# Performance work log

Measured on AMD Instinct MI355X. Metric: run time of the kernel, lower is better.

Reference implementation:

```python
import jax, jax.numpy as jnp
import numpy as np


def deform_conv2d(x, w, offset, mask, pad):
    """Modulated deformable conv (DCNv2), stride 1, dilation 1, groups 1.
    x: [B,C,H,W], w: [Co,C,kh,kw], offset: [B,2*K,H,W] (y,x per tap), mask: [B,K,H,W].
    Output spatial size equals input (pad = (k-1)//2).
    """
    B, C, H, W = x.shape
    Co, _, kh, kw = w.shape
    K = kh * kw
    off = offset.reshape(B, K, 2, H, W)
    dy, dx = off[:, :, 0], off[:, :, 1]               # [B,K,H,W]
    ky, kx = jnp.meshgrid(jnp.arange(kh), jnp.arange(kw), indexing='ij')
    ky = ky.reshape(K).astype(x.dtype)
    kx = kx.reshape(K).astype(x.dtype)
    hh = jnp.arange(H, dtype=x.dtype)
    ww = jnp.arange(W, dtype=x.dtype)
    # sampling coords: p0 + p_k + delta p_k
    py = hh[None, None, :, None] - pad + ky[None, :, None, None] + dy  # [B,K,H,W]
    px = ww[None, None, None, :] - pad + kx[None, :, None, None] + dx
    y0 = jnp.floor(py)
    x0 = jnp.floor(px)
    wy = py - y0
    wx = px - x0
    y0i = y0.astype(jnp.int32)
    x0i = x0.astype(jnp.int32)
    x_flat = x.reshape(B, C, H * W)

    def gather(yi, xi):
        valid = (yi >= 0) & (yi < H) & (xi >= 0) & (xi < W)  # zero padding outside
        idx = jnp.clip(yi, 0, H - 1) * W + jnp.clip(xi, 0, W - 1)
        g = jnp.take_along_axis(x_flat, idx.reshape(B, 1, K * H * W), axis=2)
        g = g.reshape(B, C, K, H, W)
        return g * valid[:, None].astype(x.dtype)

    v00 = gather(y0i, x0i)
    v01 = gather(y0i, x0i + 1)
    v10 = gather(y0i + 1, x0i)
    v11 = gather(y0i + 1, x0i + 1)
    wy_ = wy[:, None]  # [B,1,K,H,W]
    wx_ = wx[:, None]
    samp = (v00 * (1 - wy_) * (1 - wx_) + v01 * (1 - wy_) * wx_
            + v10 * wy_ * (1 - wx_) + v11 * wy_ * wx_)   # [B,C,K,H,W]
    # masked weighted accumulation == conv over sampled taps
    return jnp.einsum('bckhw,bkhw,ock->bohw', samp, mask, w.reshape(Co, C, K))


def setup_inputs() -> dict:
    key = jax.random.key(0)
    ks = jax.random.split(key, 10)
    B, C, H, W, Co = 4, 64, 64, 64, 64
    inp = {
        'x': jax.random.normal(ks[0], (B, C, H, W), dtype=jnp.float32),
        'filter1': jax.random.normal(ks[1], (Co, C, 3, 3), dtype=jnp.float32) * 0.05,
        'offset1': jax.random.normal(ks[2], (B, 2 * 9, H, W), dtype=jnp.float32),
        'mask1': jax.random.uniform(ks[3], (B, 9, H, W), dtype=jnp.float32),
        'filter2': jax.random.normal(ks[4], (Co, C, 5, 5), dtype=jnp.float32) * 0.03,
        'offset2': jax.random.normal(ks[5], (B, 2 * 25, H, W), dtype=jnp.float32),
        'mask2': jax.random.uniform(ks[6], (B, 25, H, W), dtype=jnp.float32),
        'filter3': jax.random.normal(ks[7], (Co, C, 7, 7), dtype=jnp.float32) * 0.02,
        'offset3': jax.random.normal(ks[8], (B, 2 * 49, H, W), dtype=jnp.float32),
        'mask3': jax.random.uniform(ks[9], (B, 49, H, W), dtype=jnp.float32),
    }
    return inp


def reference(x, filter1, offset1, mask1, filter2, offset2, mask2, filter3, offset3, mask3):
    part1 = deform_conv2d(x, filter1, offset1, mask1, pad=1)  # 3x3
    part2 = deform_conv2d(x, filter2, offset2, mask2, pad=2)  # 5x5
    part3 = deform_conv2d(x, filter3, offset3, mask3, pad=3)  # 7x7
    return jnp.concatenate((part1, part2, part3), axis=1)
```

## Files before the change

kernel.cpp:

```cpp
#include <hip/hip_runtime.h>
#include <hip/hip_bf16.h>


typedef __attribute__((ext_vector_type(8))) short bf16x8;
typedef __attribute__((ext_vector_type(8))) unsigned short u16x8;
typedef __attribute__((ext_vector_type(4))) float f32x4;
typedef __attribute__((ext_vector_type(2))) float f32x2;

#define WR 16
#define WC 30
#define WS 68
#define SLS 20

__device__ __forceinline__ unsigned short f2bf(float f) {
    __hip_bfloat16 h = __float2bfloat16(f);
    return *reinterpret_cast<unsigned short*>(&h);
}
__device__ __forceinline__ f32x2 unpk(unsigned u) {
    f32x2 r;
    r[0] = __uint_as_float(u << 16);
    r[1] = __uint_as_float(u & 0xffff0000u);
    return r;
}

__global__ __launch_bounds__(256) void k_prep(
    const float* __restrict__ x,
    const float* __restrict__ f1, const float* __restrict__ f2, const float* __restrict__ f3,
    unsigned short* __restrict__ xTb,
    unsigned short* __restrict__ wp1, unsigned short* __restrict__ wp2, unsigned short* __restrict__ wp3) {
    __shared__ float tile[64][65];
    int bid = blockIdx.x;
    int tid = threadIdx.x;
    if (bid < 256) {
        int b = bid >> 6, h = bid & 63;
        {
            int w = tid & 63, c4 = tid >> 6;
            const float* xp = x + (((b * 64) * 64 + h) * 64) + w;
            #pragma unroll
            for (int i = 0; i < 16; ++i) {
                int c = c4 * 16 + i;
                tile[c][w] = xp[c * 4096];
            }
        }
        __syncthreads();
        {
            int c = tid & 63, w4 = tid >> 6;
            unsigned short* op = xTb + (((b * 64 + h) * 64) * 64) + c;
            #pragma unroll
            for (int i = 0; i < 16; ++i) {
                int ww = w4 * 16 + i;
                op[ww * 64] = f2bf(tile[c][ww]);
            }
        }
    } else {
        int idx = (bid - 256) * 256 + tid;
        const float* f; unsigned short* wp; int K, rel;
        if (idx < 36864)       { f = f1; wp = wp1; K = 9;  rel = idx; }
        else if (idx < 139264) { f = f2; wp = wp2; K = 25; rel = idx - 36864; }
        else                   { f = f3; wp = wp3; K = 49; rel = idx - 139264; }
        int k    = rel >> 12;
        int r2   = rel & 4095;
        int ct   = r2 >> 10;
        int cg   = (r2 >> 9) & 1;
        int lane = (r2 >> 3) & 63;
        int j    = r2 & 7;
        int o = ct * 16 + (lane & 15);
        int c = cg * 32 + (lane >> 4) * 8 + j;
        wp[rel] = f2bf(f[(o * 64 + c) * K + k]);
    }
}

__global__ __launch_bounds__(512, 2) void k_dcn(
    const unsigned short* __restrict__ xTb,
    const float* __restrict__ off1, const float* __restrict__ msk1, const unsigned short* __restrict__ wp1,
    const float* __restrict__ off2, const float* __restrict__ msk2, const unsigned short* __restrict__ wp2,
    const float* __restrict__ off3, const float* __restrict__ msk3, const unsigned short* __restrict__ wp3,
    float* __restrict__ out) {

    __shared__ __align__(16) unsigned char smem[WR * WC * WS * 2];
    unsigned short* win = (unsigned short*)smem;
    float* slab = (float*)smem;

    int tile = blockIdx.x;
    int b  = tile >> 8;
    int h  = (tile >> 2) & 63;
    int w0 = (tile & 3) << 4;

    int tid  = threadIdx.x;
    int wv   = tid >> 6;
    int lane = tid & 63;
    int quad = lane >> 4;
    int l16  = lane & 15;
    int ylo  = h - 7, cxlo = w0 - 7;

    const unsigned short* xb = xTb + ((size_t)b << 18);

    int pw   = w0 + l16;
    int ch0  = quad << 3;
    int lofs = lane << 3;

    const float* offs; const float* msks; const unsigned short* wpF;
    int ks, ke, kw, pad;
    switch (wv) {
        case 0:  offs = off1; msks = msk1; wpF = wp1; kw = 3; pad = 1; ks = 0;  ke = 9;  break;
        case 1:  offs = off2; msks = msk2; wpF = wp2; kw = 5; pad = 2; ks = 0;  ke = 12; break;
        case 2:  offs = off2; msks = msk2; wpF = wp2; kw = 5; pad = 2; ks = 12; ke = 25; break;
        case 3:  offs = off3; msks = msk3; wpF = wp3; kw = 7; pad = 3; ks = 0;  ke = 10; break;
        case 4:  offs = off3; msks = msk3; wpF = wp3; kw = 7; pad = 3; ks = 10; ke = 20; break;
        case 5:  offs = off3; msks = msk3; wpF = wp3; kw = 7; pad = 3; ks = 20; ke = 30; break;
        case 6:  offs = off3; msks = msk3; wpF = wp3; kw = 7; pad = 3; ks = 30; ke = 40; break;
        default: offs = off3; msks = msk3; wpF = wp3; kw = 7; pad = 3; ks = 40; ke = 49; break;
    }
    int K2 = (kw == 3) ? 9 : (kw == 5) ? 25 : 49;
    const float* offp = offs + ((b * 2 * K2) * 4096) + (h << 6) + pw;
    const float* mskp = msks + ((b * K2) * 4096) + (h << 6) + pw;

    int kp1 = min(ks + 1, ke - 1), kp2 = min(ks + 2, ke - 1);
    float dyA = offp[ks * 8192], dxA = offp[ks * 8192 + 4096], mkA = mskp[ks * 4096];
    float dyB = offp[kp1 * 8192], dxB = offp[kp1 * 8192 + 4096], mkB = mskp[kp1 * 4096];
    float dyC = offp[kp2 * 8192], dxC = offp[kp2 * 8192 + 4096], mkC = mskp[kp2 * 4096];

    {
        int j = tid & 7;
        for (int p = tid >> 3; p < WR * WC; p += 64) {
            int r = p / WC, cc = p - r * WC;
            int y = min(max(ylo + r, 0), 63);
            int x = min(max(cxlo + cc, 0), 63);
            *(u16x8*)(win + p * WS + j * 8) =
                *(const u16x8*)(xb + (((y << 6) + x) << 6) + j * 8);
        }
    }
    __syncthreads();

    f32x4 acc[4];
    #pragma unroll
    for (int i = 0; i < 4; ++i) acc[i] = (f32x4){0.f, 0.f, 0.f, 0.f};

    int ky = ks / kw, kx = ks - ky * kw;

    for (int k = ks; k < ke; ++k) {
        const unsigned short* wpk = wpF + (k << 12) + lofs;
        bf16x8 b00 = *(const bf16x8*)(wpk);
        bf16x8 b01 = *(const bf16x8*)(wpk + 512);
        bf16x8 b10 = *(const bf16x8*)(wpk + 1024);
        bf16x8 b11 = *(const bf16x8*)(wpk + 1536);
        bf16x8 b20 = *(const bf16x8*)(wpk + 2048);
        bf16x8 b21 = *(const bf16x8*)(wpk + 2560);
        bf16x8 b30 = *(const bf16x8*)(wpk + 3072);
        bf16x8 b31 = *(const bf16x8*)(wpk + 3584);

        int kn = min(k + 3, ke - 1);
        float dyN = offp[kn * 8192];
        float dxN = offp[kn * 8192 + 4096];
        float mkN = mskp[kn * 4096];

        float py = (float)(h - pad + ky) + dyA;
        float px = (float)(pw - pad + kx) + dxA;
        float y0f = floorf(py), x0f = floorf(px);
        float wy = py - y0f, wx = px - x0f;
        int y0 = (int)y0f, x0 = (int)x0f;
        int y1 = y0 + 1, x1 = x0 + 1;
        float fy0 = ((unsigned)y0 < 64u) ? (1.f - wy) * mkA : 0.f;
        float fy1 = ((unsigned)y1 < 64u) ? wy * mkA         : 0.f;
        float gx0 = ((unsigned)x0 < 64u) ? (1.f - wx)       : 0.f;
        float gx1 = ((unsigned)x1 < 64u) ? wx               : 0.f;
        float w00 = fy0 * gx0, w01 = fy0 * gx1, w10 = fy1 * gx0, w11 = fy1 * gx1;

        int r0 = y0 - ylo, r1 = r0 + 1;
        int c0 = x0 - cxlo, c1 = c0 + 1;
        bool oow = ((w00 != 0.f) & (((unsigned)r0 >= WR) | ((unsigned)c0 >= WC)))
                 | ((w01 != 0.f) & (((unsigned)r0 >= WR) | ((unsigned)c1 >= WC)))
                 | ((w10 != 0.f) & (((unsigned)r1 >= WR) | ((unsigned)c0 >= WC)))
                 | ((w11 != 0.f) & (((unsigned)r1 >= WR) | ((unsigned)c1 >= WC)));
        int r0c = min(max(r0, 0), WR - 1), r1c = min(max(r1, 0), WR - 1);
        int c0c = min(max(c0, 0), WC - 1), c1c = min(max(c1, 0), WC - 1);
        int p00 = (r0c * WC + c0c) * WS;
        int p01 = (r0c * WC + c1c) * WS;
        int p10 = (r1c * WC + c0c) * WS;
        int p11 = (r1c * WC + c1c) * WS;

        union U { u16x8 v; unsigned u[4]; };
        U g00a, g01a, g10a, g11a, g00b, g01b, g10b, g11b;
        g00a.v = *(const u16x8*)(win + p00 + ch0);
        g01a.v = *(const u16x8*)(win + p01 + ch0);
        g10a.v = *(const u16x8*)(win + p10 + ch0);
        g11a.v = *(const u16x8*)(win + p11 + ch0);
        g00b.v = *(const u16x8*)(win + p00 + 32 + ch0);
        g01b.v = *(const u16x8*)(win + p01 + 32 + ch0);
        g10b.v = *(const u16x8*)(win + p10 + 32 + ch0);
        g11b.v = *(const u16x8*)(win + p11 + 32 + ch0);

        if (oow) {
            int y0g = min(max(y0, 0), 63), y1g = min(max(y1, 0), 63);
            int x0g = min(max(x0, 0), 63), x1g = min(max(x1, 0), 63);
            int o00 = ((y0g << 6) + x0g) << 6;
            int o01 = ((y0g << 6) + x1g) << 6;
            int o10 = ((y1g << 6) + x0g) << 6;
            int o11 = ((y1g << 6) + x1g) << 6;
            g00a.v = *(const u16x8*)(xb + o00 + ch0);
            g01a.v = *(const u16x8*)(xb + o01 + ch0);
            g10a.v = *(const u16x8*)(xb + o10 + ch0);
            g11a.v = *(const u16x8*)(xb + o11 + ch0);
            g00b.v = *(const u16x8*)(xb + o00 + 32 + ch0);
            g01b.v = *(const u16x8*)(xb + o01 + 32 + ch0);
            g10b.v = *(const u16x8*)(xb + o10 + 32 + ch0);
            g11b.v = *(const u16x8*)(xb + o11 + 32 + ch0);
        }

        f32x2 W00 = {w00, w00}, W01 = {w01, w01}, W10 = {w10, w10}, W11 = {w11, w11};
        union { bf16x8 v; unsigned short u[8]; } A0, A1;
        #pragma unroll
        for (int j2 = 0; j2 < 4; ++j2) {
            f32x2 s0 = W00 * unpk(g00a.u[j2]) + W01 * unpk(g01a.u[j2])
                     + W10 * unpk(g10a.u[j2]) + W11 * unpk(g11a.u[j2]);
            f32x2 s1 = W00 * unpk(g00b.u[j2]) + W01 * unpk(g01b.u[j2])
                     + W10 * unpk(g10b.u[j2]) + W11 * unpk(g11b.u[j2]);
            A0.u[2 * j2]     = f2bf(s0[0]);
            A0.u[2 * j2 + 1] = f2bf(s0[1]);
            A1.u[2 * j2]     = f2bf(s1[0]);
            A1.u[2 * j2 + 1] = f2bf(s1[1]);
        }

        acc[0] = __builtin_amdgcn_mfma_f32_16x16x32_bf16(A0.v, b00, acc[0], 0, 0, 0);
        acc[0] = __builtin_amdgcn_mfma_f32_16x16x32_bf16(A1.v, b01, acc[0], 0, 0, 0);
        acc[1] = __builtin_amdgcn_mfma_f32_16x16x32_bf16(A0.v, b10, acc[1], 0, 0, 0);
        acc[1] = __builtin_amdgcn_mfma_f32_16x16x32_bf16(A1.v, b11, acc[1], 0, 0, 0);
        acc[2] = __builtin_amdgcn_mfma_f32_16x16x32_bf16(A0.v, b20, acc[2], 0, 0, 0);
        acc[2] = __builtin_amdgcn_mfma_f32_16x16x32_bf16(A1.v, b21, acc[2], 0, 0, 0);
        acc[3] = __builtin_amdgcn_mfma_f32_16x16x32_bf16(A0.v, b30, acc[3], 0, 0, 0);
        acc[3] = __builtin_amdgcn_mfma_f32_16x16x32_bf16(A1.v, b31, acc[3], 0, 0, 0);

        dyA = dyB; dyB = dyC; dyC = dyN;
        dxA = dxB; dxB = dxC; dxC = dxN;
        mkA = mkB; mkB = mkC; mkC = mkN;
        if (++kx == kw) { kx = 0; ++ky; }
    }

    __syncthreads();

    #pragma unroll
    for (int ct = 0; ct < 4; ++ct) {
        *(f32x4*)&slab[wv * 1280 + (ct * 16 + l16) * SLS + quad * 4] = acc[ct];
    }
    __syncthreads();

    for (int it = tid; it < 768; it += 512) {
        int g = it & 3;
        int o = it >> 2;
        int oo = o & 63;
        int base = oo * SLS + g * 4;
        f32x4 v;
        if (o < 64) {
            v = *(const f32x4*)&slab[base];
        } else if (o < 128) {
            f32x4 a0 = *(const f32x4*)&slab[1 * 1280 + base];
            f32x4 a1 = *(const f32x4*)&slab[2 * 1280 + base];
            #pragma unroll
            for (int r = 0; r < 4; ++r) v[r] = a0[r] + a1[r];
        } else {
            f32x4 a0 = *(const f32x4*)&slab[3 * 1280 + base];
            f32x4 a1 = *(const f32x4*)&slab[4 * 1280 + base];
            f32x4 a2 = *(const f32x4*)&slab[5 * 1280 + base];
            f32x4 a3 = *(const f32x4*)&slab[6 * 1280 + base];
            f32x4 a4 = *(const f32x4*)&slab[7 * 1280 + base];
            #pragma unroll
            for (int r = 0; r < 4; ++r) v[r] = (a0[r] + a1[r]) + (a2[r] + a3[r]) + a4[r];
        }
        *(f32x4*)&out[(((size_t)b * 192 + o) * 64 + h) * 64 + w0 + g * 4] = v;
    }
}

extern "C" void kernel_launch(void* const* d_in, const int* in_sizes, int n_in,
                              void* d_out, int out_size, void* d_ws, size_t ws_size,
                              hipStream_t stream) {
    const float* x    = (const float*)d_in[0];
    const float* f1   = (const float*)d_in[1];
    const float* off1 = (const float*)d_in[2];
    const float* msk1 = (const float*)d_in[3];
    const float* f2   = (const float*)d_in[4];
    const float* off2 = (const float*)d_in[5];
    const float* msk2 = (const float*)d_in[6];
    const float* f3   = (const float*)d_in[7];
    const float* off3 = (const float*)d_in[8];
    const float* msk3 = (const float*)d_in[9];
    float* out = (float*)d_out;

    unsigned short* xTb = (unsigned short*)d_ws;
    unsigned short* wp1 = xTb + 4 * 64 * 64 * 64;
    unsigned short* wp2 = wp1 + 9 * 4096;
    unsigned short* wp3 = wp2 + 25 * 4096;

    k_prep<<<dim3(1584), dim3(256), 0, stream>>>(x, f1, f2, f3, xTb, wp1, wp2, wp3);
    k_dcn<<<dim3(1024), dim3(512), 0, stream>>>(xTb,
                                                off1, msk1, wp1,
                                                off2, msk2, wp2,
                                                off3, msk3, wp3,
                                                out);
}
```

Before: 168.9 us.

## Gather bilinear samples directly from global memory instead of staging an LDS window

Drops the per-block shared-memory staging of a 16x30 pixel window of the input, along with its barrier and the out-of-window fallback path. All four bilinear corners are now loaded straight from the bf16 channels-last input and rely on L1/L2 caching. The block's LDS footprint shrinks to the reduction slab, and launch bounds now request 8 blocks per CU to raise occupancy. The trade is more global or cache gather traffic per tap, plus a possibly tighter register budget that could cause spills.

```diff
diff --git a/kernel.cpp b/kernel.cpp
--- a/kernel.cpp
+++ b/kernel.cpp
@@ -7,9 +7,6 @@
 typedef __attribute__((ext_vector_type(4))) float f32x4;
 typedef __attribute__((ext_vector_type(2))) float f32x2;
 
-#define WR 16
-#define WC 30
-#define WS 68
 #define SLS 20
 
 __device__ __forceinline__ unsigned short f2bf(float f) {
@@ -70,16 +67,14 @@
     }
 }
 
-__global__ __launch_bounds__(512, 2) void k_dcn(
+__global__ __launch_bounds__(512, 8) void k_dcn(
     const unsigned short* __restrict__ xTb,
     const float* __restrict__ off1, const float* __restrict__ msk1, const unsigned short* __restrict__ wp1,
     const float* __restrict__ off2, const float* __restrict__ msk2, const unsigned short* __restrict__ wp2,
     const float* __restrict__ off3, const float* __restrict__ msk3, const unsigned short* __restrict__ wp3,
     float* __restrict__ out) {
 
-    __shared__ __align__(16) unsigned char smem[WR * WC * WS * 2];
-    unsigned short* win = (unsigned short*)smem;
-    float* slab = (float*)smem;
+    __shared__ __align__(16) float slab[8 * 1280];
 
     int tile = blockIdx.x;
     int b  = tile >> 8;
@@ -91,7 +86,6 @@
     int lane = tid & 63;
     int quad = lane >> 4;
     int l16  = lane & 15;
-    int ylo  = h - 7, cxlo = w0 - 7;
 
     const unsigned short* xb = xTb + ((size_t)b << 18);
 
@@ -120,18 +114,6 @@
     float dyB = offp[kp1 * 8192], dxB = offp[kp1 * 8192 + 4096], mkB = mskp[kp1 * 4096];
     float dyC = offp[kp2 * 8192], dxC = offp[kp2 * 8192 + 4096], mkC = mskp[kp2 * 4096];
 
-    {
-        int j = tid & 7;
-        for (int p = tid >> 3; p < WR * WC; p += 64) {
-            int r = p / WC, cc = p - r * WC;
-            int y = min(max(ylo + r, 0), 63);
-            int x = min(max(cxlo + cc, 0), 63);
-            *(u16x8*)(win + p * WS + j * 8) =
-                *(const u16x8*)(xb + (((y << 6) + x) << 6) + j * 8);
-        }
-    }
-    __syncthreads();
-
     f32x4 acc[4];
     #pragma unroll
     for (int i = 0; i < 4; ++i) acc[i] = (f32x4){0.f, 0.f, 0.f, 0.f};
@@ -166,46 +148,23 @@
         float gx1 = ((unsigned)x1 < 64u) ? wx               : 0.f;
         float w00 = fy0 * gx0, w01 = fy0 * gx1, w10 = fy1 * gx0, w11 = fy1 * gx1;
 
-        int r0 = y0 - ylo, r1 = r0 + 1;
-        int c0 = x0 - cxlo, c1 = c0 + 1;
-        bool oow = ((w00 != 0.f) & (((unsigned)r0 >= WR) | ((unsigned)c0 >= WC)))
-                 | ((w01 != 0.f) & (((unsigned)r0 >= WR) | ((unsigned)c1 >= WC)))
-                 | ((w10 != 0.f) & (((unsigned)r1 >= WR) | ((unsigned)c0 >= WC)))
-                 | ((w11 != 0.f) & (((unsigned)r1 >= WR) | ((unsigned)c1 >= WC)));
-        int r0c = min(max(r0, 0), WR - 1), r1c = min(max(r1, 0), WR - 1);
-        int c0c = min(max(c0, 0), WC - 1), c1c = min(max(c1, 0), WC - 1);
-        int p00 = (r0c * WC + c0c) * WS;
-        int p01 = (r0c * WC + c1c) * WS;
-        int p10 = (r1c * WC + c0c) * WS;
-        int p11 = (r1c * WC + c1c) * WS;
+        int y0g = min(max(y0, 0), 63), y1g = min(max(y1, 0), 63);
+        int x0g = min(max(x0, 0), 63), x1g = min(max(x1, 0), 63);
+        int o00 = ((y0g << 6) + x0g) << 6;
+        int o01 = ((y0g << 6) + x1g) << 6;
+        int o10 = ((y1g << 6) + x0g) << 6;
+        int o11 = ((y1g << 6) + x1g) << 6;
 
         union U { u16x8 v; unsigned u[4]; };
         U g00a, g01a, g10a, g11a, g00b, g01b, g10b, g11b;
-        g00a.v = *(const u16x8*)(win + p00 + ch0);
-        g01a.v = *(const u16x8*)(win + p01 + ch0);
-        g10a.v = *(const u16x8*)(win + p10 + ch0);
-        g11a.v = *(const u16x8*)(win + p11 + ch0);
-        g00b.v = *(const u16x8*)(win + p00 + 32 + ch0);
-        g01b.v = *(const u16x8*)(win + p01 + 32 + ch0);
-        g10b.v = *(const u16x8*)(win + p10 + 32 + ch0);
-        g11b.v = *(const u16x8*)(win + p11 + 32 + ch0);
-
-        if (oow) {
-            int y0g = min(max(y0, 0), 63), y1g = min(max(y1, 0), 63);
-            int x0g = min(max(x0, 0), 63), x1g = min(max(x1, 0), 63);
-            int o00 = ((y0g << 6) + x0g) << 6;
-            int o01 = ((y0g << 6) + x1g) << 6;
-            int o10 = ((y1g << 6) + x0g) << 6;
-            int o11 = ((y1g << 6) + x1g) << 6;
-            g00a.v = *(const u16x8*)(xb + o00 + ch0);
-            g01a.v = *(const u16x8*)(xb + o01 + ch0);
-            g10a.v = *(const u16x8*)(xb + o10 + ch0);
-            g11a.v = *(const u16x8*)(xb + o11 + ch0);
-            g00b.v = *(const u16x8*)(xb + o00 + 32 + ch0);
-            g01b.v = *(const u16x8*)(xb + o01 + 32 + ch0);
-            g10b.v = *(const u16x8*)(xb + o10 + 32 + ch0);
-            g11b.v = *(const u16x8*)(xb + o11 + 32 + ch0);
-        }
+        g00a.v = *(const u16x8*)(xb + o00 + ch0);
+        g01a.v = *(const u16x8*)(xb + o01 + ch0);
+        g10a.v = *(const u16x8*)(xb + o10 + ch0);
+        g11a.v = *(const u16x8*)(xb + o11 + ch0);
+        g00b.v = *(const u16x8*)(xb + o00 + 32 + ch0);
+        g01b.v = *(const u16x8*)(xb + o01 + 32 + ch0);
+        g10b.v = *(const u16x8*)(xb + o10 + 32 + ch0);
+        g11b.v = *(const u16x8*)(xb + o11 + 32 + ch0);
 
         f32x2 W00 = {w00, w00}, W01 = {w01, w01}, W10 = {w10, w10}, W11 = {w11, w11};
         union { bf16x8 v; unsigned short u[8]; } A0, A1;
@@ -235,8 +194,6 @@
         mkA = mkB; mkB = mkC; mkC = mkN;
         if (++kx == kw) { kx = 0; ++ky; }
     }
-
-    __syncthreads();
 
     #pragma unroll
     for (int ct = 0; ct < 4; ++ct) {
```

Result: slower. 302.9 us (+79.3%).
